# Kernel optimization log

Hardware: AMD Instinct MI355X
Metric: run time of the kernel (lower is better)

Reference implementation:

```python
import jax, jax.numpy as jnp
import numpy as np

IN_CH = 256
QK_CH = IN_CH // 8  # 32

def setup_inputs() -> dict:
    key = jax.random.key(0)
    ks = jax.random.split(key, 7)
    x = jax.random.normal(ks[0], (4, IN_CH, 64, 64), dtype=jnp.float32)
    s_in = 1.0 / np.sqrt(IN_CH)
    # 1x1 conv weights stored as [out_ch, in_ch]; biases [out_ch]
    Wq = jax.random.uniform(ks[1], (QK_CH, IN_CH), jnp.float32, -s_in, s_in)
    bq = jax.random.uniform(ks[2], (QK_CH,), jnp.float32, -s_in, s_in)
    Wk = jax.random.uniform(ks[3], (QK_CH, IN_CH), jnp.float32, -s_in, s_in)
    bk = jax.random.uniform(ks[4], (QK_CH,), jnp.float32, -s_in, s_in)
    Wv = jax.random.uniform(ks[5], (IN_CH, IN_CH), jnp.float32, -s_in, s_in)
    bv = jax.random.uniform(ks[6], (IN_CH,), jnp.float32, -s_in, s_in)
    return {"x": x, "Wq": Wq, "bq": bq, "Wk": Wk, "bk": bk, "Wv": Wv, "bv": bv}

def reference(x, Wq, bq, Wk, bk, Wv, bv):
    n, c, h, w = x.shape
    xf = x.reshape(n, c, h * w)  # [n, c, hw]
    # 1x1 convs == per-position channel matmuls
    q = jnp.einsum('oc,ncs->nos', Wq, xf) + bq[None, :, None]  # [n, c/8, hw]
    k = jnp.einsum('oc,ncs->nos', Wk, xf) + bk[None, :, None]  # [n, c/8, hw]
    v = jnp.einsum('oc,ncs->nos', Wv, xf) + bv[None, :, None]  # [n, c,  hw]
    # energy[n, i, j] = <q[:, i], k[:, j]>  (no scaling, as in original)
    energy = jnp.einsum('nci,ncj->nij', q, k)  # [n, hw, hw]
    attention = jax.nn.softmax(energy, axis=-1)
    # out[n, c, i] = sum_j v[n, c, j] * attention[n, i, j]
    out = jnp.einsum('ncj,nij->nci', v, attention)
    return out.reshape(n, c, h, w)
```

## Files before the change

kernel.cpp:

```cpp
#include <hip/hip_runtime.h>
#include <hip/hip_bf16.h>
#include <stdint.h>
#include <stddef.h>

typedef unsigned short u16;
typedef unsigned int   u32;
typedef __attribute__((ext_vector_type(8))) short bf16x8;
typedef __attribute__((ext_vector_type(4))) float f32x4;

#define LOG2E   1.44269504f
#define EXP_OFF 23.0831206f

static __device__ __forceinline__ float bf2f(u16 v) {
    u32 u = ((u32)v) << 16; float f; __builtin_memcpy(&f, &u, 4); return f;
}
static __device__ __forceinline__ u16 f2bf(float f) {
    u32 u; __builtin_memcpy(&u, &f, 4);
    u32 r = (u + 0x7fffu + ((u >> 16) & 1u)) >> 16; return (u16)r;
}
static __device__ __forceinline__ float as_f(u32 u) { float f; __builtin_memcpy(&f, &u, 4); return f; }
static __device__ __forceinline__ u32   as_u(float f) { u32 u; __builtin_memcpy(&u, &f, 4); return u; }

static __device__ __forceinline__ int detect_f32_wave0(const void* x, int t) {
    const u32* xw = (const u32*)x;
    int bad = 0;
    #pragma unroll
    for (int k = 0; k < 4; ++k) {
        u32 wv = xw[(t << 2) + k];
        int e = (wv >> 7) & 0xff;
        bad += (e >= 160);
    }
    unsigned long long m = __ballot(bad > 0);
    return (__popcll(m) >= 8) ? 1 : 0;
}


__global__ __launch_bounds__(256) void qkv_proj_mfma(
    const void* __restrict__ x,
    const void* __restrict__ Wq, const void* __restrict__ bq,
    const void* __restrict__ Wk, const void* __restrict__ bk,
    const void* __restrict__ Wv, const void* __restrict__ bv,
    u16* __restrict__ qws, u16* __restrict__ kws, u16* __restrict__ vws,
    int n_off, int nshiftp)
{
    __shared__ u16 Wl[64 * 256];
    __shared__ int dtf;

    const int t    = threadIdx.x;
    const int bid  = blockIdx.x;
    const int n_w  = bid & ((1 << nshiftp) - 1);
    const int rest = bid >> nshiftp;
    const int g    = rest % 5;
    const int it   = rest / 5;
    const int n_g  = n_off + n_w;
    const int i0   = it << 6;

    if (t < 64) { int f = detect_f32_wave0(x, t); if (t == 0) dtf = f; }
    __syncthreads();
    const bool isf32 = (dtf != 0);

    #pragma unroll
    for (int k = 0; k < 16; ++k) {
        int idx  = t + (k << 8);
        int row  = idx >> 6;
        int col4 = (idx & 63) << 2;
        const void* src; int srow;
        if (g == 0) {
            if (row < 32) { src = Wq; srow = row; }
            else          { src = Wk; srow = row - 32; }
        } else { src = Wv; srow = ((g - 1) << 6) + row; }
        ushort4 h;
        if (isf32) {
            float4 wv = *((const float4*)((const float*)src + srow * 256 + col4));
            h.x = f2bf(wv.x); h.y = f2bf(wv.y); h.z = f2bf(wv.z); h.w = f2bf(wv.w);
        } else {
            h = *((const ushort4*)((const u16*)src + srow * 256 + col4));
        }
        *(ushort4*)&Wl[(row << 8) + (col4 ^ ((row & 7) << 3))] = h;
    }
    __syncthreads();

    const int lane = t & 63;
    const int w    = t >> 6;
    const int n16  = lane & 15;
    const int quad = lane >> 4;
    const int i_b  = i0 + (w << 4);
    const int i    = i_b + n16;
    const int swz  = (n16 & 7) << 3;

    f32x4 acc[4];
    #pragma unroll
    for (int f = 0; f < 4; ++f) acc[f] = (f32x4){0.f, 0.f, 0.f, 0.f};

    if (isf32) {
        const float* xp = (const float*)x
            + (((size_t)(n_g * 256 + (quad << 3))) << 12) + i;
        float af[8];
        #pragma unroll
        for (int e = 0; e < 8; ++e) af[e] = xp[(size_t)e << 12];
        #pragma unroll
        for (int c8 = 0; c8 < 8; ++c8) {
            bf16x8 a;
            #pragma unroll
            for (int e = 0; e < 8; ++e) a[e] = (short)f2bf(af[e]);
            if (c8 < 7) {
                const float* xn = xp + (((size_t)(c8 + 1) << 5) << 12);
                #pragma unroll
                for (int e = 0; e < 8; ++e) af[e] = xn[(size_t)e << 12];
            }
            const int c0 = c8 << 5;
            #pragma unroll
            for (int f = 0; f < 4; ++f) {
                const int brow = (f << 4) + n16;
                bf16x8 b = *(const bf16x8*)
                    &Wl[(brow << 8) + ((c0 + (quad << 3)) ^ swz)];
                acc[f] = __builtin_amdgcn_mfma_f32_16x16x32_bf16(a, b, acc[f], 0, 0, 0);
            }
        }
    } else {
        const u16* xp = (const u16*)x
            + (((size_t)(n_g * 256 + (quad << 3))) << 12) + i;
        u16 af[8];
        #pragma unroll
        for (int e = 0; e < 8; ++e) af[e] = xp[(size_t)e << 12];
        #pragma unroll
        for (int c8 = 0; c8 < 8; ++c8) {
            bf16x8 a;
            #pragma unroll
            for (int e = 0; e < 8; ++e) a[e] = (short)af[e];
            if (c8 < 7) {
                const u16* xn = xp + (((size_t)(c8 + 1) << 5) << 12);
                #pragma unroll
                for (int e = 0; e < 8; ++e) af[e] = xn[(size_t)e << 12];
            }
            const int c0 = c8 << 5;
            #pragma unroll
            for (int f = 0; f < 4; ++f) {
                const int brow = (f << 4) + n16;
                bf16x8 b = *(const bf16x8*)
                    &Wl[(brow << 8) + ((c0 + (quad << 3)) ^ swz)];
                acc[f] = __builtin_amdgcn_mfma_f32_16x16x32_bf16(a, b, acc[f], 0, 0, 0);
            }
        }
    }

    if (g == 0) {
        #pragma unroll
        for (int f = 0; f < 4; ++f) {
            const int ol   = (f << 4) + n16;
            const bool isq = (ol < 32);
            const int och  = isq ? ol : (ol - 32);
            float bias;
            if (isf32) bias = ((const float*)(isq ? bq : bk))[och];
            else       bias = bf2f(((const u16*)(isq ? bq : bk))[och]);
            u16* dst = (isq ? qws : kws) + (((size_t)n_w) << 17) + och;
            const float scale = isq ? LOG2E : 1.0f;
            #pragma unroll
            for (int r = 0; r < 4; ++r) {
                const int ii = i_b + (quad << 2) + r;
                dst[(size_t)ii << 5] = f2bf((acc[f][r] + bias) * scale);
            }
        }
    } else {
        #pragma unroll
        for (int f = 0; f < 4; ++f) {
            const int c = ((g - 1) << 6) + (f << 4) + n16;
            float bias = isf32 ? ((const float*)bv)[c]
                               : bf2f(((const u16*)bv)[c]);
            const int i4 = i_b + (quad << 2);
            ushort4 h;
            h.x = f2bf(acc[f][0] + bias);
            h.y = f2bf(acc[f][1] + bias);
            h.z = f2bf(acc[f][2] + bias);
            h.w = f2bf(acc[f][3] + bias);
            const size_t addr = ((size_t)n_w << 20)
                + ((size_t)(c >> 4) << 16)
                + ((size_t)(i4 >> 5) << 9)
                + (size_t)((((((i4 & 31) >> 3) << 4) + (c & 15)) << 3) + (i4 & 7));
            *(ushort4*)(vws + addr) = h;
        }
    }
}

__global__ __launch_bounds__(1024) void flash_mfma10(
    const u16* __restrict__ qws, const u16* __restrict__ kws,
    const u16* __restrict__ vws, void* __restrict__ out,
    const void* __restrict__ x, int n_off, int nshift)
{
    __shared__ __align__(16) char arena[17920];
    __shared__ __align__(16) float lS[64];
    __shared__ int dtf;
    u16*   PsA  = (u16*)arena;
    float* Dbuf = (float*)arena;

    const int t    = threadIdx.x;
    const int lane = t & 63;
    const int w    = t >> 6;
    const int n16  = lane & 15;
    const int quad = lane >> 4;
    const int bid  = blockIdx.x;
    const int n_w  = bid & ((1 << nshift) - 1);
    const int qt   = bid >> nshift;
    const int n_g  = n_off + n_w;
    const int i0   = qt << 6;

    if (t < 64) {
        int f = detect_f32_wave0(x, t);
        if (t == 0) dtf = f;
        lS[t] = 0.f;
    }

    const u16* qb = qws + (((size_t)n_w) << 17);
    const u16* kb = kws + (((size_t)n_w) << 17);
    const u16* vb = vws + (((size_t)n_w) << 20);

    const int qsub_s = w & 3;
    const int jsub   = w >> 2;
    const int qh = w & 1;
    const int cg = (w >> 1) & 3;
    const int jh = w >> 3;

    const bf16x8 qfrag =
        *(const bf16x8*)(qb + ((size_t)(i0 + (qsub_s << 4) + n16) << 5) + (quad << 3));

    f32x4 acc[2][4];
    #pragma unroll
    for (int a = 0; a < 2; ++a)
        #pragma unroll
        for (int b = 0; b < 4; ++b) acc[a][b] = (f32x4){0.f, 0.f, 0.f, 0.f};
    float lp[4] = {0.f, 0.f, 0.f, 0.f};

    const int jcol = (jsub << 4) + n16;
    const int j8   = jcol >> 3;
    const int jlo  = jcol & 7;
    const int ksw  = (jh << 2) + quad;
    const f32x4 zoff = {-EXP_OFF, -EXP_OFF, -EXP_OFF, -EXP_OFF};

    const u16* kp = kb + ((size_t)((jsub << 4) + n16) << 5) + (quad << 3);
    const u16* vfp[4];
    #pragma unroll
    for (int cf = 0; cf < 4; ++cf)
        vfp[cf] = vb + ((size_t)((cg << 2) + cf) << 16) + ((size_t)jh << 9)
                     + ((size_t)((quad << 4) + n16) << 3);

    bf16x8 kcur, knext, vf[4];

    kcur = *(const bf16x8*)(kp);
    {
        u16* Ps = PsA;
        f32x4 s = __builtin_amdgcn_mfma_f32_16x16x32_bf16(qfrag, kcur, zoff, 0, 0, 0);
        #pragma unroll
        for (int r = 0; r < 4; ++r) {
            const int qrow = (qsub_s << 4) + (quad << 2) + r;
            float p = exp2f(s[r]);
            u32 u = as_u(p) & 0xffff0000u;
            lp[r] += as_f(u);
            Ps[qrow * 64 + ((j8 ^ (qrow & 7)) << 3) + jlo] = (u16)(u >> 16);
        }
        knext = *(const bf16x8*)(kp + 2048);
        #pragma unroll
        for (int cf = 0; cf < 4; ++cf)
            vf[cf] = *(const bf16x8*)(vfp[cf]);
    }
    __syncthreads();

    for (int tile = 1; tile < 64; ++tile) {
        const int par  = tile & 1;
        u16* Psc = PsA + (par << 12);
        u16* Psp = PsA + ((par ^ 1) << 12);

        kcur = knext;
        if (tile < 63) {
            knext = *(const bf16x8*)(kp + ((size_t)(tile + 1) << 11));
        }

        bf16x8 pa[2];
        #pragma unroll
        for (int qs = 0; qs < 2; ++qs) {
            const int qrow = (qh << 5) + (qs << 4) + n16;
            pa[qs] = *(const bf16x8*)&Psp[qrow * 64 + ((ksw ^ (qrow & 7)) << 3)];
        }
        #pragma unroll
        for (int qs = 0; qs < 2; ++qs)
            #pragma unroll
            for (int cf = 0; cf < 4; ++cf)
                acc[qs][cf] = __builtin_amdgcn_mfma_f32_16x16x32_bf16(
                    pa[qs], vf[cf], acc[qs][cf], 0, 0, 0);

        #pragma unroll
        for (int cf = 0; cf < 4; ++cf)
            vf[cf] = *(const bf16x8*)(vfp[cf] + ((size_t)tile << 10));

        f32x4 s = __builtin_amdgcn_mfma_f32_16x16x32_bf16(qfrag, kcur, zoff, 0, 0, 0);
        #pragma unroll
        for (int r = 0; r < 4; ++r) {
            const int qrow = (qsub_s << 4) + (quad << 2) + r;
            float p = exp2f(s[r]);
            u32 u = as_u(p) & 0xffff0000u;
            lp[r] += as_f(u);
            Psc[qrow * 64 + ((j8 ^ (qrow & 7)) << 3) + jlo] = (u16)(u >> 16);
        }

        __syncthreads();
    }

    {
        u16* Psp = PsA + (1 << 12);
        bf16x8 pa[2];
        #pragma unroll
        for (int qs = 0; qs < 2; ++qs) {
            const int qrow = (qh << 5) + (qs << 4) + n16;
            pa[qs] = *(const bf16x8*)&Psp[qrow * 64 + ((ksw ^ (qrow & 7)) << 3)];
        }
        #pragma unroll
        for (int qs = 0; qs < 2; ++qs)
            #pragma unroll
            for (int cf = 0; cf < 4; ++cf)
                acc[qs][cf] = __builtin_amdgcn_mfma_f32_16x16x32_bf16(
                    pa[qs], vf[cf], acc[qs][cf], 0, 0, 0);
    }

    #pragma unroll
    for (int r = 0; r < 4; ++r) {
        lp[r] += __shfl_xor(lp[r], 1);
        lp[r] += __shfl_xor(lp[r], 2);
        lp[r] += __shfl_xor(lp[r], 4);
        lp[r] += __shfl_xor(lp[r], 8);
    }
    if (n16 == 0) {
        #pragma unroll
        for (int r = 0; r < 4; ++r)
            atomicAdd(&lS[(qsub_s << 4) + (quad << 2) + r], lp[r]);
    }
    __syncthreads();
    if (t < 64) lS[t] = 1.0f / lS[t];
    const bool isf32 = (dtf != 0);

    for (int chunk = 0; chunk < 4; ++chunk) {
        __syncthreads();
        if (jh == 1 && cg == chunk) {
            #pragma unroll
            for (int qs = 0; qs < 2; ++qs)
                #pragma unroll
                for (int cf = 0; cf < 4; ++cf)
                    *(f32x4*)&Dbuf[((cf << 4) + n16) * 68 +
                                   (qh << 5) + (qs << 4) + (quad << 2)] = acc[qs][cf];
        }
        __syncthreads();
        if (jh == 0 && cg == chunk) {
            #pragma unroll
            for (int qs = 0; qs < 2; ++qs)
                #pragma unroll
                for (int cf = 0; cf < 4; ++cf) {
                    float* p = &Dbuf[((cf << 4) + n16) * 68 +
                                     (qh << 5) + (qs << 4) + (quad << 2)];
                    f32x4 d = *(f32x4*)p;
                    d += acc[qs][cf];
                    *(f32x4*)p = d;
                }
        }
        __syncthreads();
        const int c_l = t >> 4;
        const int qg  = (t & 15) << 2;
        float4 d  = *(float4*)&Dbuf[c_l * 68 + qg];
        float4 rl = *(float4*)&lS[qg];
        const int c_glob = (chunk << 6) + c_l;
        const size_t ob = (((size_t)(n_g * 256 + c_glob)) << 12) + i0 + qg;
        if (isf32) {
            float4 o = make_float4(d.x * rl.x, d.y * rl.y, d.z * rl.z, d.w * rl.w);
            *(float4*)((float*)out + ob) = o;
        } else {
            union { uint2 v; u16 h[4]; } o;
            o.h[0] = f2bf(d.x * rl.x);
            o.h[1] = f2bf(d.y * rl.y);
            o.h[2] = f2bf(d.z * rl.z);
            o.h[3] = f2bf(d.w * rl.w);
            *(uint2*)((u16*)out + ob) = o.v;
        }
    }
}

extern "C" void kernel_launch(void* const* d_in, const int* in_sizes, int n_in,
                              void* d_out, int out_size, void* d_ws, size_t ws_size,
                              hipStream_t stream)
{
    const void* x  = d_in[0];
    const void* Wq = d_in[1];
    const void* bq = d_in[2];
    const void* Wk = d_in[3];
    const void* bk = d_in[4];
    const void* Wv = d_in[5];
    const void* bv = d_in[6];

    const size_t full_need = (size_t)(4u * 4096u) * (32 + 32 + 256) * 2;
    if (ws_size >= full_need) {
        u16* qws = (u16*)d_ws;
        u16* kws = qws + (size_t)4 * 4096 * 32;
        u16* vws = kws + (size_t)4 * 4096 * 32;
        qkv_proj_mfma<<<dim3(1280), dim3(256), 0, stream>>>(
            x, Wq, bq, Wk, bk, Wv, bv, qws, kws, vws, 0, 2);
        flash_mfma10<<<dim3(256), dim3(1024), 0, stream>>>(
            qws, kws, vws, d_out, x, 0, 2);
    } else {
        u16* qws = (u16*)d_ws;
        u16* kws = qws + (size_t)4096 * 32;
        u16* vws = kws + (size_t)4096 * 32;
        for (int n = 0; n < 4; ++n) {
            qkv_proj_mfma<<<dim3(320), dim3(256), 0, stream>>>(
                x, Wq, bq, Wk, bk, Wv, bv, qws, kws, vws, n, 0);
            flash_mfma10<<<dim3(64), dim3(1024), 0, stream>>>(
                qws, kws, vws, d_out, x, n, 0);
        }
    }
}
```

Measured before the change: 149.8 us.

## Repartition PV matmul across waves with 16x16x16 MFMA and new V layout

Changes how the 16 waves split the P·V product. Each wave now covers all 64 query rows for one channel group and a quarter of the key tile, using 16x16x16 bf16 MFMAs with 4-element fragments. Before, each wave covered 32 rows and half the key tile with 16x16x32 MFMAs. The V workspace layout and the P shared-memory swizzle are rewritten to match. The aim is to reuse each V fragment across more query rows and cut V global loads per wave, at the cost of twice as many accumulator registers and a longer four-way cross-wave reduction at the end.

```diff
diff --git a/kernel.cpp b/kernel.cpp
--- a/kernel.cpp
+++ b/kernel.cpp
@@ -6,6 +6,7 @@
 typedef unsigned short u16;
 typedef unsigned int   u32;
 typedef __attribute__((ext_vector_type(8))) short bf16x8;
+typedef __attribute__((ext_vector_type(4))) short bf16x4;
 typedef __attribute__((ext_vector_type(4))) float f32x4;
 
 #define LOG2E   1.44269504f
@@ -20,6 +21,10 @@
 }
 static __device__ __forceinline__ float as_f(u32 u) { float f; __builtin_memcpy(&f, &u, 4); return f; }
 static __device__ __forceinline__ u32   as_u(float f) { u32 u; __builtin_memcpy(&u, &f, 4); return u; }
+
+static __device__ __forceinline__ void mfma16(f32x4& d, bf16x4 a, bf16x4 b) {
+    asm("v_mfma_f32_16x16x16_bf16 %0, %1, %2, %0" : "+v"(d) : "v"(a), "v"(b));
+}
 
 static __device__ __forceinline__ int detect_f32_wave0(const void* x, int t) {
     const u32* xw = (const u32*)x;
@@ -175,14 +180,14 @@
             h.w = f2bf(acc[f][3] + bias);
             const size_t addr = ((size_t)n_w << 20)
                 + ((size_t)(c >> 4) << 16)
-                + ((size_t)(i4 >> 5) << 9)
-                + (size_t)((((((i4 & 31) >> 3) << 4) + (c & 15)) << 3) + (i4 & 7));
+                + ((size_t)(i4 >> 4) << 8)
+                + (size_t)((((i4 >> 2) & 3) << 6) + ((c & 15) << 2));
             *(ushort4*)(vws + addr) = h;
         }
     }
 }
 
-__global__ __launch_bounds__(1024) void flash_mfma10(
+__global__ __launch_bounds__(1024) void flash_mfma14(
     const u16* __restrict__ qws, const u16* __restrict__ kws,
     const u16* __restrict__ vws, void* __restrict__ out,
     const void* __restrict__ x, int n_off, int nshift)
@@ -190,7 +195,7 @@
     __shared__ __align__(16) char arena[17920];
     __shared__ __align__(16) float lS[64];
     __shared__ int dtf;
-    u16*   PsA  = (u16*)arena;
+    char*  PsA  = arena;
     float* Dbuf = (float*)arena;
 
     const int t    = threadIdx.x;
@@ -216,16 +221,15 @@
 
     const int qsub_s = w & 3;
     const int jsub   = w >> 2;
-    const int qh = w & 1;
-    const int cg = (w >> 1) & 3;
-    const int jh = w >> 3;
+    const int cg = w & 3;
+    const int js = w >> 2;
 
     const bf16x8 qfrag =
         *(const bf16x8*)(qb + ((size_t)(i0 + (qsub_s << 4) + n16) << 5) + (quad << 3));
 
-    f32x4 acc[2][4];
-    #pragma unroll
-    for (int a = 0; a < 2; ++a)
+    f32x4 acc[4][4];
+    #pragma unroll
+    for (int a = 0; a < 4; ++a)
         #pragma unroll
         for (int b = 0; b < 4; ++b) acc[a][b] = (f32x4){0.f, 0.f, 0.f, 0.f};
     float lp[4] = {0.f, 0.f, 0.f, 0.f};
@@ -233,91 +237,95 @@
     const int jcol = (jsub << 4) + n16;
     const int j8   = jcol >> 3;
     const int jlo  = jcol & 7;
-    const int ksw  = (jh << 2) + quad;
     const f32x4 zoff = {-EXP_OFF, -EXP_OFF, -EXP_OFF, -EXP_OFF};
+
+    int pwoff[4];
+    #pragma unroll
+    for (int r = 0; r < 4; ++r) {
+        const int qrow = (qsub_s << 4) + (quad << 2) + r;
+        const int gw = j8 ^ (qrow & 7) ^ (((qrow >> 3) & 1) << 2);
+        pwoff[r] = qrow * 128 + (gw << 4) + (jlo << 1);
+    }
+    int paoff[4];
+    #pragma unroll
+    for (int qs = 0; qs < 4; ++qs) {
+        const int q  = (qs << 4) + n16;
+        const int gr = ((js << 1) + (quad >> 1)) ^ (n16 & 7) ^ ((n16 >> 3) << 2);
+        paoff[qs] = q * 128 + (gr << 4) + ((quad & 1) << 3);
+    }
 
     const u16* kp = kb + ((size_t)((jsub << 4) + n16) << 5) + (quad << 3);
     const u16* vfp[4];
     #pragma unroll
     for (int cf = 0; cf < 4; ++cf)
-        vfp[cf] = vb + ((size_t)((cg << 2) + cf) << 16) + ((size_t)jh << 9)
-                     + ((size_t)((quad << 4) + n16) << 3);
-
-    bf16x8 kcur, knext, vf[4];
+        vfp[cf] = vb + ((size_t)((cg << 2) + cf) << 16) + ((size_t)js << 8)
+                     + (size_t)((quad << 6) + (n16 << 2));
+
+    bf16x8 kcur, knext;
+    bf16x4 vf[4];
 
     kcur = *(const bf16x8*)(kp);
     {
-        u16* Ps = PsA;
         f32x4 s = __builtin_amdgcn_mfma_f32_16x16x32_bf16(qfrag, kcur, zoff, 0, 0, 0);
         #pragma unroll
         for (int r = 0; r < 4; ++r) {
-            const int qrow = (qsub_s << 4) + (quad << 2) + r;
             float p = exp2f(s[r]);
             u32 u = as_u(p) & 0xffff0000u;
             lp[r] += as_f(u);
-            Ps[qrow * 64 + ((j8 ^ (qrow & 7)) << 3) + jlo] = (u16)(u >> 16);
+            *(u16*)(PsA + pwoff[r]) = (u16)(u >> 16);
         }
         knext = *(const bf16x8*)(kp + 2048);
         #pragma unroll
         for (int cf = 0; cf < 4; ++cf)
-            vf[cf] = *(const bf16x8*)(vfp[cf]);
+            vf[cf] = *(const bf16x4*)(vfp[cf]);
     }
     __syncthreads();
 
     for (int tile = 1; tile < 64; ++tile) {
-        const int par  = tile & 1;
-        u16* Psc = PsA + (par << 12);
-        u16* Psp = PsA + ((par ^ 1) << 12);
+        const int par = tile & 1;
+        char* Psc = PsA + (par << 13);
+        char* Psp = PsA + ((par ^ 1) << 13);
 
         kcur = knext;
-        if (tile < 63) {
-            knext = *(const bf16x8*)(kp + ((size_t)(tile + 1) << 11));
-        }
-
-        bf16x8 pa[2];
-        #pragma unroll
-        for (int qs = 0; qs < 2; ++qs) {
-            const int qrow = (qh << 5) + (qs << 4) + n16;
-            pa[qs] = *(const bf16x8*)&Psp[qrow * 64 + ((ksw ^ (qrow & 7)) << 3)];
-        }
-        #pragma unroll
-        for (int qs = 0; qs < 2; ++qs)
+        if (tile < 63) knext = *(const bf16x8*)(kp + ((size_t)(tile + 1) << 11));
+
+        bf16x4 pa[4];
+        #pragma unroll
+        for (int qs = 0; qs < 4; ++qs)
+            pa[qs] = *(const bf16x4*)(Psp + paoff[qs]);
+        #pragma unroll
+        for (int qs = 0; qs < 4; ++qs)
             #pragma unroll
             for (int cf = 0; cf < 4; ++cf)
-                acc[qs][cf] = __builtin_amdgcn_mfma_f32_16x16x32_bf16(
-                    pa[qs], vf[cf], acc[qs][cf], 0, 0, 0);
+                mfma16(acc[qs][cf], pa[qs], vf[cf]);
 
         #pragma unroll
         for (int cf = 0; cf < 4; ++cf)
-            vf[cf] = *(const bf16x8*)(vfp[cf] + ((size_t)tile << 10));
+            vf[cf] = *(const bf16x4*)(vfp[cf] + ((size_t)tile << 10));
 
         f32x4 s = __builtin_amdgcn_mfma_f32_16x16x32_bf16(qfrag, kcur, zoff, 0, 0, 0);
         #pragma unroll
         for (int r = 0; r < 4; ++r) {
-            const int qrow = (qsub_s << 4) + (quad << 2) + r;
             float p = exp2f(s[r]);
             u32 u = as_u(p) & 0xffff0000u;
             lp[r] += as_f(u);
-            Psc[qrow * 64 + ((j8 ^ (qrow & 7)) << 3) + jlo] = (u16)(u >> 16);
+            *(u16*)(Psc + pwoff[r]) = (u16)(u >> 16);
         }
 
         __syncthreads();
     }
 
     {
-        u16* Psp = PsA + (1 << 12);
-        bf16x8 pa[2];
-        #pragma unroll
-        for (int qs = 0; qs < 2; ++qs) {
-            const int qrow = (qh << 5) + (qs << 4) + n16;
-            pa[qs] = *(const bf16x8*)&Psp[qrow * 64 + ((ksw ^ (qrow & 7)) << 3)];
-        }
-        #pragma unroll
-        for (int qs = 0; qs < 2; ++qs)
+        char* Psp = PsA + 8192;
+        bf16x4 pa[4];
+        #pragma unroll
+        for (int qs = 0; qs < 4; ++qs)
+            pa[qs] = *(const bf16x4*)(Psp + paoff[qs]);
+        #pragma unroll
+        for (int qs = 0; qs < 4; ++qs)
             #pragma unroll
             for (int cf = 0; cf < 4; ++cf)
-                acc[qs][cf] = __builtin_amdgcn_mfma_f32_16x16x32_bf16(
-                    pa[qs], vf[cf], acc[qs][cf], 0, 0, 0);
+                mfma16(acc[qs][cf], pa[qs], vf[cf]);
     }
 
     #pragma unroll
@@ -338,26 +346,29 @@
 
     for (int chunk = 0; chunk < 4; ++chunk) {
         __syncthreads();
-        if (jh == 1 && cg == chunk) {
-            #pragma unroll
-            for (int qs = 0; qs < 2; ++qs)
+        if (cg == chunk && js == 0) {
+            #pragma unroll
+            for (int qs = 0; qs < 4; ++qs)
                 #pragma unroll
                 for (int cf = 0; cf < 4; ++cf)
                     *(f32x4*)&Dbuf[((cf << 4) + n16) * 68 +
-                                   (qh << 5) + (qs << 4) + (quad << 2)] = acc[qs][cf];
-        }
-        __syncthreads();
-        if (jh == 0 && cg == chunk) {
-            #pragma unroll
-            for (int qs = 0; qs < 2; ++qs)
+                                   (qs << 4) + (quad << 2)] = acc[qs][cf];
+        }
+        #pragma unroll
+        for (int jsrc = 1; jsrc < 4; ++jsrc) {
+            __syncthreads();
+            if (cg == chunk && js == jsrc) {
                 #pragma unroll
-                for (int cf = 0; cf < 4; ++cf) {
-                    float* p = &Dbuf[((cf << 4) + n16) * 68 +
-                                     (qh << 5) + (qs << 4) + (quad << 2)];
-                    f32x4 d = *(f32x4*)p;
-                    d += acc[qs][cf];
-                    *(f32x4*)p = d;
-                }
+                for (int qs = 0; qs < 4; ++qs)
+                    #pragma unroll
+                    for (int cf = 0; cf < 4; ++cf) {
+                        float* p = &Dbuf[((cf << 4) + n16) * 68 +
+                                         (qs << 4) + (quad << 2)];
+                        f32x4 d = *(f32x4*)p;
+                        d += acc[qs][cf];
+                        *(f32x4*)p = d;
+                    }
+            }
         }
         __syncthreads();
         const int c_l = t >> 4;
@@ -399,7 +410,7 @@
         u16* vws = kws + (size_t)4 * 4096 * 32;
         qkv_proj_mfma<<<dim3(1280), dim3(256), 0, stream>>>(
             x, Wq, bq, Wk, bk, Wv, bv, qws, kws, vws, 0, 2);
-        flash_mfma10<<<dim3(256), dim3(1024), 0, stream>>>(
+        flash_mfma14<<<dim3(256), dim3(1024), 0, stream>>>(
             qws, kws, vws, d_out, x, 0, 2);
     } else {
         u16* qws = (u16*)d_ws;
@@ -408,7 +419,7 @@
         for (int n = 0; n < 4; ++n) {
             qkv_proj_mfma<<<dim3(320), dim3(256), 0, stream>>>(
                 x, Wq, bq, Wk, bk, Wv, bv, qws, kws, vws, n, 0);
-            flash_mfma10<<<dim3(64), dim3(1024), 0, stream>>>(
+            flash_mfma14<<<dim3(64), dim3(1024), 0, stream>>>(
                 qws, kws, vws, d_out, x, n, 0);
         }
     }
```

Result: slower. 163.6 us (+9.2%).
